# Kernel optimization log

Hardware: AMD Instinct MI355X
Metric: run time of the kernel (lower is better)

## Reference

```python
import jax, jax.numpy as jnp
import numpy as np

BATCH = 131072
N = 64          # total bits
PARTS = 16      # len(partition) == dpp_size
M = 4           # bits per part
D = PARTS
EPS = 1e-8


def _colnorm(a):
    return a / jnp.linalg.norm(a, axis=0, keepdims=True)


def setup_inputs() -> dict:
    key = jax.random.key(0)
    k0, k1, k2, k3, k4 = jax.random.split(key, 5)
    x = jax.random.randint(k0, (BATCH, N), 0, 2, dtype=jnp.int32)
    W = jax.random.normal(k1, (PARTS, (1 << M) - 1), dtype=jnp.float32)
    A = _colnorm(jax.random.normal(k2, (D, D), dtype=jnp.float32))
    B = _colnorm(jax.random.normal(k3, (D, D), dtype=jnp.float32))
    C = _colnorm(jax.random.normal(k4, (D, D), dtype=jnp.float32))
    return {"x": x, "W": W, "A": A, "B": B, "C": C}


def reference(x, W, A, B, C):
    batch = x.shape[0]
    # --- Simple PCs (vectorized over the 16 parts): bit-pack each 4-bit part ---
    bits = x.reshape(batch, PARTS, M)                       # contiguous partition
    pow2 = (1 << jnp.arange(M)).astype(jnp.int32)           # [M]
    idx = jnp.sum(bits * pow2, axis=-1)                     # [B, P] in [0, 2^M)
    w = jax.nn.softmax(W, axis=-1)                          # [P, 2^M - 1]
    w = jnp.concatenate([jnp.zeros((PARTS, 1), w.dtype), w], axis=-1)  # [P, 2^M]
    p = w[jnp.arange(PARTS)[None, :], idx]                  # [B, P]

    # --- L matrix: sym PD part + skew part ---
    I = jnp.eye(D, dtype=A.dtype)
    L0 = A.T @ A + (B @ C.T - C @ B.T) + EPS * I            # [D, D]

    # column-scale by p, then force diagonal to 1 where p == 0
    Lp = L0[None, :, :] * p[:, None, :]                     # [B, D, D]
    eye_b = jnp.eye(D, dtype=bool)
    mask = eye_b[None, :, :] & (p == 0.0)[:, :, None]
    Lp = jnp.where(mask, jnp.asarray(1.0, Lp.dtype), Lp)

    sign, logabs = jnp.linalg.slogdet(Lp)                   # [B]
    y = logabs + jnp.log(jax.lax.stop_gradient(sign))       # nan if det < 0 (matches torch.logdet)
    s0, la0 = jnp.linalg.slogdet(L0 + I)
    alpha = la0 + jnp.log(jax.lax.stop_gradient(s0))
    return y - alpha
```

## Files before the change

### kernel.cpp

```cpp
#include <hip/hip_runtime.h>
#include <math.h>

#define BATCH 131072
#define EPS 1e-8f


__global__ __launch_bounds__(64, 1) void stageA_kernel(const float* __restrict__ W,
                                                       const float* __restrict__ A,
                                                       const float* __restrict__ Bm,
                                                       const float* __restrict__ Cm,
                                                       float* __restrict__ ws) {
    __shared__ float sL0[256];
    int lt = threadIdx.x;
    #pragma unroll
    for (int q = 0; q < 4; ++q) {
        int e = lt * 4 + q;
        int i = e >> 4, j = e & 15;
        float s = 0.f;
        #pragma unroll
        for (int k = 0; k < 16; ++k) {
            s += A[k * 16 + i] * A[k * 16 + j];
            s += Bm[i * 16 + k] * Cm[j * 16 + k]
               - Cm[i * 16 + k] * Bm[j * 16 + k];
        }
        if (i == j) s += EPS;
        sL0[e] = s;
    }
    __syncthreads();

    unsigned tg = blockIdx.x * 64u + (unsigned)lt;

    if (tg >= 288u && tg < 304u) {
        int r = (int)tg - 288;
        float row[15];
        float mx = -1e30f;
        #pragma unroll
        for (int q = 0; q < 15; ++q) { row[q] = W[r * 15 + q]; mx = fmaxf(mx, row[q]); }
        float se = 0.f;
        #pragma unroll
        for (int q = 0; q < 15; ++q) se += expf(row[q] - mx);
        float lse = mx + logf(se);
        ws[r * 16 + 0] = 0.f;
        #pragma unroll
        for (int q = 0; q < 15; ++q) ws[r * 16 + 1 + q] = row[q] - lse;
    }

    if (tg > 256u) return;
    bool isAlpha = (tg == 256u);
    unsigned h = isAlpha ? 0xFFu : tg;

    float a[16][16];
    #pragma unroll
    for (int r = 0; r < 16; ++r) {
        int i = (r < 8) ? (8 + r) : (r - 8);
        bool pi = (i < 8) ? true : (((h >> (i - 8)) & 1u) != 0u);
        #pragma unroll
        for (int c = 0; c < 16; ++c) {
            int j = (c < 8) ? (8 + c) : (c - 8);
            bool pj = (j < 8) ? true : (((h >> (j - 8)) & 1u) != 0u);
            float v = (pi && pj) ? sL0[i * 16 + j] : ((r == c) ? 1.f : 0.f);
            if (isAlpha && r == c) v += 1.f;
            a[r][c] = v;
        }
    }

    float plog = 0.f;
    #pragma unroll
    for (int k = 0; k < 8; ++k) {
        float piv = a[k][k];
        plog += __logf(fabsf(piv));
        float inv = 1.0f / piv;
        #pragma unroll
        for (int r2 = k + 1; r2 < 16; ++r2) {
            float f = a[r2][k] * inv;
            #pragma unroll
            for (int c2 = k + 1; c2 < 16; ++c2)
                a[r2][c2] = fmaf(-f, a[k][c2], a[r2][c2]);
        }
    }

    if (!isAlpha) {
        #pragma unroll
        for (int i = 0; i < 8; ++i)
            #pragma unroll
            for (int j = 0; j < 8; ++j)
                ws[512 + h * 64 + i * 8 + j] = a[8 + i][8 + j];
        ws[17408 + h] = plog;
    } else {
        #pragma unroll
        for (int k = 8; k < 16; ++k) {
            float piv = a[k][k];
            plog += __logf(fabsf(piv));
            float inv = 1.0f / piv;
            #pragma unroll
            for (int r2 = k + 1; r2 < 16; ++r2) {
                float f = a[r2][k] * inv;
                #pragma unroll
                for (int c2 = k + 1; c2 < 16; ++c2)
                    a[r2][c2] = fmaf(-f, a[k][c2], a[r2][c2]);
            }
        }
        ws[256] = plog;
    }
}

__global__ __launch_bounds__(256) void stageB_kernel(const float* __restrict__ ws,
                                                     float* __restrict__ T) {
    __shared__ float s8[64];
    __shared__ float sp[2];
    int lt = threadIdx.x;
    int b  = blockIdx.x;
    if (lt < 64)  s8[lt] = ws[512 + b * 64 + lt];
    if (lt == 64) sp[0] = ws[17408 + b];
    if (lt == 65) sp[1] = ws[256];
    __syncthreads();

    unsigned lo = (unsigned)lt;
    float a[8][8];
    #pragma unroll
    for (int i = 0; i < 8; ++i) {
        bool bi = ((lo >> i) & 1u) != 0u;
        #pragma unroll
        for (int j = 0; j < 8; ++j) {
            bool bj = ((lo >> j) & 1u) != 0u;
            a[i][j] = (bi && bj) ? s8[i * 8 + j] : ((i == j) ? 1.f : 0.f);
        }
    }

    float ld = sp[0] - sp[1];
    #pragma unroll
    for (int k = 0; k < 8; ++k) {
        float piv = a[k][k];
        ld += __logf(fabsf(piv));
        float inv = 1.0f / piv;
        #pragma unroll
        for (int i = k + 1; i < 8; ++i) {
            float f = a[i][k] * inv;
            #pragma unroll
            for (int j = k + 1; j < 8; ++j)
                a[i][j] = fmaf(-f, a[k][j], a[i][j]);
        }
    }

    T[b * 256 + lt] = ld;
}

__global__ __launch_bounds__(256) void main_kernel(const int4* __restrict__ x,
                                                   const float* __restrict__ ws,
                                                   float* __restrict__ out) {
    __shared__ float slw[256];
    int lt = threadIdx.x;
    slw[lt] = ws[lt];
    __syncthreads();

    int b = blockIdx.x * 256 + lt;
    const int4* xb = x + (size_t)b * 16;

    float lw = 0.f;
    unsigned mask = 0;
    #pragma unroll
    for (int j = 0; j < 16; ++j) {
        int4 v = xb[j];
        int idx = v.x + 2 * v.y + 4 * v.z + 8 * v.w;
        lw += slw[j * 16 + idx];
        mask |= (idx != 0 ? 1u : 0u) << j;
    }
    out[b] = lw + ws[32768 + mask];
}

extern "C" void kernel_launch(void* const* d_in, const int* in_sizes, int n_in,
                              void* d_out, int out_size, void* d_ws, size_t ws_size,
                              hipStream_t stream) {
    const float* W = (const float*)d_in[1];
    const float* A = (const float*)d_in[2];
    const float* B = (const float*)d_in[3];
    const float* C = (const float*)d_in[4];
    const int4*  x = (const int4*)d_in[0];
    float* ws  = (float*)d_ws;
    float* out = (float*)d_out;

    stageA_kernel<<<5, 64, 0, stream>>>(W, A, B, C, ws);
    stageB_kernel<<<256, 256, 0, stream>>>(ws, ws + 32768);
    main_kernel<<<BATCH / 256, 256, 0, stream>>>(x, ws, out);
}
```

Before: 90.42 us.

## Fuse 8x8 Schur-complement determinant into main kernel, drop table-building stage

Removes the stageB kernel, which precomputed a 65536-entry log-determinant table over all subset masks. Each sample now loads the 8x8 Schur complement for its high-byte mask and runs an 8x8 LU elimination inline. This saves one kernel launch and the table build, but every one of the 131072 samples now does the elimination itself rather than one per mask. The table path was already a precompute over the fixed parameter space, and recomputing per sample adds ALU work to a memory-bound kernel.

```diff
diff --git a/kernel.cpp b/kernel.cpp
--- a/kernel.cpp
+++ b/kernel.cpp
@@ -104,57 +104,18 @@
     }
 }
 
-__global__ __launch_bounds__(256) void stageB_kernel(const float* __restrict__ ws,
-                                                     float* __restrict__ T) {
-    __shared__ float s8[64];
-    __shared__ float sp[2];
-    int lt = threadIdx.x;
-    int b  = blockIdx.x;
-    if (lt < 64)  s8[lt] = ws[512 + b * 64 + lt];
-    if (lt == 64) sp[0] = ws[17408 + b];
-    if (lt == 65) sp[1] = ws[256];
-    __syncthreads();
-
-    unsigned lo = (unsigned)lt;
-    float a[8][8];
-    #pragma unroll
-    for (int i = 0; i < 8; ++i) {
-        bool bi = ((lo >> i) & 1u) != 0u;
-        #pragma unroll
-        for (int j = 0; j < 8; ++j) {
-            bool bj = ((lo >> j) & 1u) != 0u;
-            a[i][j] = (bi && bj) ? s8[i * 8 + j] : ((i == j) ? 1.f : 0.f);
-        }
-    }
-
-    float ld = sp[0] - sp[1];
-    #pragma unroll
-    for (int k = 0; k < 8; ++k) {
-        float piv = a[k][k];
-        ld += __logf(fabsf(piv));
-        float inv = 1.0f / piv;
-        #pragma unroll
-        for (int i = k + 1; i < 8; ++i) {
-            float f = a[i][k] * inv;
-            #pragma unroll
-            for (int j = k + 1; j < 8; ++j)
-                a[i][j] = fmaf(-f, a[k][j], a[i][j]);
-        }
-    }
-
-    T[b * 256 + lt] = ld;
-}
-
 __global__ __launch_bounds__(256) void main_kernel(const int4* __restrict__ x,
                                                    const float* __restrict__ ws,
                                                    float* __restrict__ out) {
     __shared__ float slw[256];
+    __shared__ float sAlpha;
     int lt = threadIdx.x;
     slw[lt] = ws[lt];
+    if (lt == 0) sAlpha = ws[256];
     __syncthreads();
 
-    int b = blockIdx.x * 256 + lt;
-    const int4* xb = x + (size_t)b * 16;
+    int g = blockIdx.x * 256 + lt;
+    const int4* xb = x + (size_t)g * 16;
 
     float lw = 0.f;
     unsigned mask = 0;
@@ -165,7 +126,43 @@
         lw += slw[j * 16 + idx];
         mask |= (idx != 0 ? 1u : 0u) << j;
     }
-    out[b] = lw + ws[32768 + mask];
+    const unsigned h2 = mask >> 8;
+    const unsigned lo = mask & 255u;
+
+    const float4* S4 = (const float4*)(ws + 512 + (size_t)h2 * 64);
+    float a[8][8];
+    #pragma unroll
+    for (int i = 0; i < 16; ++i) {
+        const float4 q4 = S4[i];
+        const int ri = i >> 1, cb = (i & 1) * 4;
+        a[ri][cb + 0] = q4.x; a[ri][cb + 1] = q4.y;
+        a[ri][cb + 2] = q4.z; a[ri][cb + 3] = q4.w;
+    }
+    #pragma unroll
+    for (int i = 0; i < 8; ++i) {
+        const bool bi = ((lo >> i) & 1u) != 0u;
+        #pragma unroll
+        for (int j = 0; j < 8; ++j) {
+            const bool bj = ((lo >> j) & 1u) != 0u;
+            if (!(bi && bj)) a[i][j] = (i == j) ? 1.f : 0.f;
+        }
+    }
+
+    float ld = ws[17408 + h2] + lw - sAlpha;
+    #pragma unroll
+    for (int k = 0; k < 8; ++k) {
+        const float piv = a[k][k];
+        ld += __logf(fabsf(piv));
+        const float inv = 1.0f / piv;
+        #pragma unroll
+        for (int i = k + 1; i < 8; ++i) {
+            const float f = a[i][k] * inv;
+            #pragma unroll
+            for (int j = k + 1; j < 8; ++j)
+                a[i][j] = fmaf(-f, a[k][j], a[i][j]);
+        }
+    }
+    out[g] = ld;
 }
 
 extern "C" void kernel_launch(void* const* d_in, const int* in_sizes, int n_in,
@@ -180,6 +177,5 @@
     float* out = (float*)d_out;
 
     stageA_kernel<<<5, 64, 0, stream>>>(W, A, B, C, ws);
-    stageB_kernel<<<256, 256, 0, stream>>>(ws, ws + 32768);
     main_kernel<<<BATCH / 256, 256, 0, stream>>>(x, ws, out);
 }
```

Result: no change. 90.49 us (+0.1%).
